# Performance work log

Measured on AMD Instinct MI355X. Metric: run time of the kernel, lower is better.

Reference implementation:

```python
import jax, jax.numpy as jnp
import numpy as np

BLOCK = 4096  # bitsandbytes blockwise-quantization block size


def setup_inputs() -> dict:
    key = jax.random.key(0)
    k_x, k_w, k_a, k_c, k_b = jax.random.split(key, 5)
    out_features, in_features = 16384, 4096
    numel = out_features * in_features
    x = jax.random.normal(k_x, (2, 2048, in_features), dtype=jnp.float32)
    # int8 codes stored as indices into the 256-entry dequant table
    qweight = jax.random.randint(k_w, (out_features, in_features), 0, 256, dtype=jnp.int32)
    absmax = jax.random.uniform(k_a, (numel // BLOCK,), dtype=jnp.float32)
    code = jax.random.normal(k_c, (256,), dtype=jnp.float32)
    bias = jax.random.normal(k_b, (out_features,), dtype=jnp.float32)
    return {"x": x, "qweight": qweight, "absmax": absmax, "code": code, "bias": bias}


def reference(x, qweight, absmax, code, bias):
    # dequantize_blockwise: w[i] = code[q[i]] * absmax[i // BLOCK]
    out_f, in_f = qweight.shape
    w = (code[qweight.reshape(-1)].reshape(-1, BLOCK) * absmax[:, None]).reshape(out_f, in_f)
    # F.linear(x, W, b) = x @ W^T + b
    return jnp.einsum("bsi,oi->bso", x, w) + bias
```

## Files before the change

kernel.cpp:

```cpp
#include <hip/hip_runtime.h>
#include <hip/hip_bf16.h>


typedef __bf16 bf16x8 __attribute__((ext_vector_type(8)));
typedef __bf16 bf16x4 __attribute__((ext_vector_type(4)));
typedef float  f32x4  __attribute__((ext_vector_type(4)));

#define GLD_LDS(gp, lp) \
    __builtin_amdgcn_global_load_lds((const __attribute__((address_space(1))) void*)(gp), \
                                     (__attribute__((address_space(3))) void*)(lp), 16, 0, 0)

static constexpr int M = 4096;
static constexpr int N = 16384;
static constexpr int K = 4096;
static constexpr int BM = 256;
static constexpr int BN = 256;
static constexpr int BK = 64;
static constexpr int NT = K / BK;
static constexpr int LDS_BYTES = 2 * 2 * 256 * BK * 2;

__global__ __launch_bounds__(256) void dequant_w(const int4* __restrict__ q4,
                                                 const float* __restrict__ code,
                                                 const float* __restrict__ absmax,
                                                 bf16x4* __restrict__ W)
{
    __shared__ float lc[256];
    lc[threadIdx.x] = code[threadIdx.x];
    __syncthreads();
    unsigned gid = blockIdx.x * 256u + threadIdx.x;
    int4 qv = q4[gid];
    float am = absmax[gid >> 10];
    bf16x4 w;
    w[0] = (__bf16)(lc[qv.x] * am);
    w[1] = (__bf16)(lc[qv.y] * am);
    w[2] = (__bf16)(lc[qv.z] * am);
    w[3] = (__bf16)(lc[qv.w] * am);
    W[gid] = w;
}

__global__ __launch_bounds__(256) void cvt_x(const float4* __restrict__ x,
                                             bf16x4* __restrict__ xb)
{
    unsigned gid = blockIdx.x * 256u + threadIdx.x;
    float4 v = x[gid];
    bf16x4 o;
    o[0] = (__bf16)v.x;
    o[1] = (__bf16)v.y;
    o[2] = (__bf16)v.z;
    o[3] = (__bf16)v.w;
    xb[gid] = o;
}


__device__ __forceinline__ void stage_half(const __bf16* gp, char* ldsbase, int h, int tid)
{
    GLD_LDS(gp + (size_t)(h * 128) * K,      ldsbase + h * 16384 +        tid * 16);
    GLD_LDS(gp + (size_t)(h * 128 + 64) * K, ldsbase + h * 16384 + 8192 + tid * 16);
}

__device__ __forceinline__ void tile_step(const __bf16*& agn, const __bf16*& bgn,
                                          const char* cA, const char* cB,
                                          char* nA, char* nB, bool pf, int tid,
                                          int baseA, int baseB, f32x4 (&acc)[8][4])
{
    if (pf) {
        stage_half(agn, nA, 0, tid);
        stage_half(agn, nA, 1, tid);
        stage_half(bgn, nB, 0, tid);
        asm volatile("s_waitcnt vmcnt(6)" ::: "memory");
    } else {
        asm volatile("s_waitcnt vmcnt(0)" ::: "memory");
    }
    __builtin_amdgcn_s_barrier();

    if (pf) {
        stage_half(bgn, nB, 1, tid);
        agn += BK;
        bgn += BK;
    }

    bf16x8 bfr[4][2], af[2][2];
#pragma unroll
    for (int ni = 0; ni < 4; ++ni) {
        bfr[ni][0] = *(const bf16x8*)(cB + (baseB + ni * 2048));
        bfr[ni][1] = *(const bf16x8*)(cB + ((baseB + ni * 2048) ^ 64));
    }
    af[0][0] = *(const bf16x8*)(cA + baseA);
    af[0][1] = *(const bf16x8*)(cA + (baseA ^ 64));
    af[1][0] = *(const bf16x8*)(cA + (baseA + 2048));
    af[1][1] = *(const bf16x8*)(cA + ((baseA + 2048) ^ 64));

    __builtin_amdgcn_s_barrier();
    __builtin_amdgcn_s_setprio(1);
#pragma unroll
    for (int kk = 0; kk < 2; ++kk)
#pragma unroll
        for (int i = 0; i < 2; ++i)
#pragma unroll
            for (int ni = 0; ni < 4; ++ni)
                acc[i][ni] = __builtin_amdgcn_mfma_f32_16x16x32_bf16(
                    af[i][kk], bfr[ni][kk], acc[i][ni], 0, 0, 0);
    __builtin_amdgcn_s_setprio(0);
    __builtin_amdgcn_s_barrier();

#pragma unroll
    for (int p = 1; p < 4; ++p) {
        af[0][0] = *(const bf16x8*)(cA + (baseA + (2 * p) * 2048));
        af[0][1] = *(const bf16x8*)(cA + ((baseA + (2 * p) * 2048) ^ 64));
        af[1][0] = *(const bf16x8*)(cA + (baseA + (2 * p + 1) * 2048));
        af[1][1] = *(const bf16x8*)(cA + ((baseA + (2 * p + 1) * 2048) ^ 64));
        __builtin_amdgcn_s_barrier();
        __builtin_amdgcn_s_setprio(1);
#pragma unroll
        for (int kk = 0; kk < 2; ++kk)
#pragma unroll
            for (int i = 0; i < 2; ++i)
#pragma unroll
                for (int ni = 0; ni < 4; ++ni)
                    acc[2 * p + i][ni] = __builtin_amdgcn_mfma_f32_16x16x32_bf16(
                        af[i][kk], bfr[ni][kk], acc[2 * p + i][ni], 0, 0, 0);
        __builtin_amdgcn_s_setprio(0);
        __builtin_amdgcn_s_barrier();
    }
}

__global__ __launch_bounds__(512, 2) void gemm_bt_bias(const __bf16* __restrict__ A,
                                                       const __bf16* __restrict__ B,
                                                       const float* __restrict__ bias,
                                                       float* __restrict__ C)
{
    extern __shared__ char lds[];
    const int tid  = threadIdx.x;
    const int lane = tid & 63;
    const int wave = tid >> 6;
    const int wm = wave >> 2;
    const int wn = wave & 3;

    const int cpx  = (int)gridDim.x >> 3;
    const int flat = ((int)blockIdx.x & 7) * cpx + ((int)blockIdx.x >> 3);
    const int bm = (flat & (M / BM - 1)) * BM;
    const int bn = (flat / (M / BM)) * BN;

    const int r0 = tid >> 3;
    const int cs = (tid & 7) ^ (r0 & 7);
    const __bf16* ag = A + (size_t)(bm + r0) * K + cs * 8;
    const __bf16* bg = B + (size_t)(bn + r0) * K + cs * 8;

    char* const ldsA0 = lds;
    char* const ldsB0 = lds + 32768;
    char* const ldsA1 = lds + 65536;
    char* const ldsB1 = lds + 98304;

    const int swz   = ((lane >> 4) ^ (lane & 7)) << 4;
    const int baseA = (wm * 128 + (lane & 15)) * 128 + swz;
    const int baseB = (wn * 64  + (lane & 15)) * 128 + swz;

    f32x4 acc[8][4] = {};

    stage_half(ag, ldsA0, 0, tid);
    stage_half(ag, ldsA0, 1, tid);
    stage_half(bg, ldsB0, 0, tid);
    stage_half(bg, ldsB0, 1, tid);

    const __bf16* agn = ag + BK;
    const __bf16* bgn = bg + BK;

    for (int t2 = 0; t2 < NT; t2 += 2) {
        tile_step(agn, bgn, ldsA0, ldsB0, ldsA1, ldsB1, true,         tid, baseA, baseB, acc);
        tile_step(agn, bgn, ldsA1, ldsB1, ldsA0, ldsB0, t2 + 2 < NT,  tid, baseA, baseB, acc);
    }

    const int cn = lane & 15;
    const int rq = (lane >> 4) * 4;
#pragma unroll
    for (int ni = 0; ni < 4; ++ni) {
        const int n = bn + wn * 64 + ni * 16 + cn;
        const float bv = bias[n];
#pragma unroll
        for (int mi = 0; mi < 8; ++mi) {
#pragma unroll
            for (int r = 0; r < 4; ++r) {
                const int m = bm + wm * 128 + mi * 16 + rq + r;
                C[(size_t)m * N + n] = acc[mi][ni][r] + bv;
            }
        }
    }
}

extern "C" void kernel_launch(void* const* d_in, const int* in_sizes, int n_in,
                              void* d_out, int out_size, void* d_ws, size_t ws_size,
                              hipStream_t stream)
{
    const float* x      = (const float*)d_in[0];
    const int*   qw     = (const int*)d_in[1];
    const float* absmax = (const float*)d_in[2];
    const float* code   = (const float*)d_in[3];
    const float* bias   = (const float*)d_in[4];
    float* out = (float*)d_out;

    __bf16* Wb = (__bf16*)d_ws;
    __bf16* Xb = (__bf16*)((char*)d_ws + (size_t)N * K * sizeof(__bf16));

    static bool attr_set = false;
    if (!attr_set) {
        (void)hipFuncSetAttribute((const void*)gemm_bt_bias,
                                  hipFuncAttributeMaxDynamicSharedMemorySize, LDS_BYTES);
        attr_set = true;
    }

    dequant_w<<<(N * (long long)K) / 4 / 256, 256, 0, stream>>>(
        (const int4*)qw, code, absmax, (bf16x4*)Wb);

    cvt_x<<<(M * (long long)K) / 4 / 256, 256, 0, stream>>>(
        (const float4*)x, (bf16x4*)Xb);

    gemm_bt_bias<<<dim3((M / BM) * (N / BN)), dim3(512), LDS_BYTES, stream>>>(
        Xb, Wb, bias, out);
}
```

Before: 1.006 ms.

## Split GEMM tile into quadrants with interleaved staging, and widen prep kernels

```diff
diff --git a/kernel.cpp b/kernel.cpp
--- a/kernel.cpp
+++ b/kernel.cpp
@@ -3,7 +3,6 @@
 
 
 typedef __bf16 bf16x8 __attribute__((ext_vector_type(8)));
-typedef __bf16 bf16x4 __attribute__((ext_vector_type(4)));
 typedef float  f32x4  __attribute__((ext_vector_type(4)));
 
 #define GLD_LDS(gp, lp) \
@@ -17,111 +16,66 @@
 static constexpr int BN = 256;
 static constexpr int BK = 64;
 static constexpr int NT = K / BK;
-static constexpr int LDS_BYTES = 2 * 2 * 256 * BK * 2;
+static constexpr int LDS_BYTES = 131072;
 
 __global__ __launch_bounds__(256) void dequant_w(const int4* __restrict__ q4,
                                                  const float* __restrict__ code,
                                                  const float* __restrict__ absmax,
-                                                 bf16x4* __restrict__ W)
+                                                 bf16x8* __restrict__ W)
 {
     __shared__ float lc[256];
     lc[threadIdx.x] = code[threadIdx.x];
     __syncthreads();
-    unsigned gid = blockIdx.x * 256u + threadIdx.x;
-    int4 qv = q4[gid];
-    float am = absmax[gid >> 10];
-    bf16x4 w;
-    w[0] = (__bf16)(lc[qv.x] * am);
-    w[1] = (__bf16)(lc[qv.y] * am);
-    w[2] = (__bf16)(lc[qv.z] * am);
-    w[3] = (__bf16)(lc[qv.w] * am);
-    W[gid] = w;
+    const unsigned total  = (unsigned)((unsigned long long)N * K / 8);
+    const unsigned stride = gridDim.x * 256u;
+    for (unsigned gid = blockIdx.x * 256u + threadIdx.x; gid < total; gid += stride) {
+        int4 q0 = q4[2u * gid];
+        int4 q1 = q4[2u * gid + 1u];
+        float am = absmax[gid >> 9];
+        bf16x8 w;
+        w[0] = (__bf16)(lc[q0.x] * am);
+        w[1] = (__bf16)(lc[q0.y] * am);
+        w[2] = (__bf16)(lc[q0.z] * am);
+        w[3] = (__bf16)(lc[q0.w] * am);
+        w[4] = (__bf16)(lc[q1.x] * am);
+        w[5] = (__bf16)(lc[q1.y] * am);
+        w[6] = (__bf16)(lc[q1.z] * am);
+        w[7] = (__bf16)(lc[q1.w] * am);
+        W[gid] = w;
+    }
 }
 
 __global__ __launch_bounds__(256) void cvt_x(const float4* __restrict__ x,
-                                             bf16x4* __restrict__ xb)
-{
-    unsigned gid = blockIdx.x * 256u + threadIdx.x;
-    float4 v = x[gid];
-    bf16x4 o;
-    o[0] = (__bf16)v.x;
-    o[1] = (__bf16)v.y;
-    o[2] = (__bf16)v.z;
-    o[3] = (__bf16)v.w;
-    xb[gid] = o;
-}
-
-
-__device__ __forceinline__ void stage_half(const __bf16* gp, char* ldsbase, int h, int tid)
-{
-    GLD_LDS(gp + (size_t)(h * 128) * K,      ldsbase + h * 16384 +        tid * 16);
-    GLD_LDS(gp + (size_t)(h * 128 + 64) * K, ldsbase + h * 16384 + 8192 + tid * 16);
-}
-
-__device__ __forceinline__ void tile_step(const __bf16*& agn, const __bf16*& bgn,
-                                          const char* cA, const char* cB,
-                                          char* nA, char* nB, bool pf, int tid,
-                                          int baseA, int baseB, f32x4 (&acc)[8][4])
-{
-    if (pf) {
-        stage_half(agn, nA, 0, tid);
-        stage_half(agn, nA, 1, tid);
-        stage_half(bgn, nB, 0, tid);
-        asm volatile("s_waitcnt vmcnt(6)" ::: "memory");
-    } else {
-        asm volatile("s_waitcnt vmcnt(0)" ::: "memory");
-    }
-    __builtin_amdgcn_s_barrier();
-
-    if (pf) {
-        stage_half(bgn, nB, 1, tid);
-        agn += BK;
-        bgn += BK;
-    }
-
-    bf16x8 bfr[4][2], af[2][2];
-#pragma unroll
-    for (int ni = 0; ni < 4; ++ni) {
-        bfr[ni][0] = *(const bf16x8*)(cB + (baseB + ni * 2048));
-        bfr[ni][1] = *(const bf16x8*)(cB + ((baseB + ni * 2048) ^ 64));
-    }
-    af[0][0] = *(const bf16x8*)(cA + baseA);
-    af[0][1] = *(const bf16x8*)(cA + (baseA ^ 64));
-    af[1][0] = *(const bf16x8*)(cA + (baseA + 2048));
-    af[1][1] = *(const bf16x8*)(cA + ((baseA + 2048) ^ 64));
-
-    __builtin_amdgcn_s_barrier();
+                                             bf16x8* __restrict__ xb)
+{
+    const unsigned total  = (unsigned)((unsigned long long)M * K / 8);
+    const unsigned stride = gridDim.x * 256u;
+    for (unsigned gid = blockIdx.x * 256u + threadIdx.x; gid < total; gid += stride) {
+        float4 a = x[2u * gid];
+        float4 b = x[2u * gid + 1u];
+        bf16x8 o;
+        o[0] = (__bf16)a.x; o[1] = (__bf16)a.y; o[2] = (__bf16)a.z; o[3] = (__bf16)a.w;
+        o[4] = (__bf16)b.x; o[5] = (__bf16)b.y; o[6] = (__bf16)b.z; o[7] = (__bf16)b.w;
+        xb[gid] = o;
+    }
+}
+
+
+template<int MH, int NH>
+__device__ __forceinline__ void mfma_quad(f32x4 (&acc)[8][4],
+                                          const bf16x8 (&af)[4][2],
+                                          const bf16x8 (&bf)[2][2])
+{
     __builtin_amdgcn_s_setprio(1);
 #pragma unroll
     for (int kk = 0; kk < 2; ++kk)
 #pragma unroll
-        for (int i = 0; i < 2; ++i)
-#pragma unroll
-            for (int ni = 0; ni < 4; ++ni)
-                acc[i][ni] = __builtin_amdgcn_mfma_f32_16x16x32_bf16(
-                    af[i][kk], bfr[ni][kk], acc[i][ni], 0, 0, 0);
+        for (int mi = 0; mi < 4; ++mi)
+#pragma unroll
+            for (int ni = 0; ni < 2; ++ni)
+                acc[MH * 4 + mi][NH * 2 + ni] = __builtin_amdgcn_mfma_f32_16x16x32_bf16(
+                    af[mi][kk], bf[ni][kk], acc[MH * 4 + mi][NH * 2 + ni], 0, 0, 0);
     __builtin_amdgcn_s_setprio(0);
-    __builtin_amdgcn_s_barrier();
-
-#pragma unroll
-    for (int p = 1; p < 4; ++p) {
-        af[0][0] = *(const bf16x8*)(cA + (baseA + (2 * p) * 2048));
-        af[0][1] = *(const bf16x8*)(cA + ((baseA + (2 * p) * 2048) ^ 64));
-        af[1][0] = *(const bf16x8*)(cA + (baseA + (2 * p + 1) * 2048));
-        af[1][1] = *(const bf16x8*)(cA + ((baseA + (2 * p + 1) * 2048) ^ 64));
-        __builtin_amdgcn_s_barrier();
-        __builtin_amdgcn_s_setprio(1);
-#pragma unroll
-        for (int kk = 0; kk < 2; ++kk)
-#pragma unroll
-            for (int i = 0; i < 2; ++i)
-#pragma unroll
-                for (int ni = 0; ni < 4; ++ni)
-                    acc[2 * p + i][ni] = __builtin_amdgcn_mfma_f32_16x16x32_bf16(
-                        af[i][kk], bfr[ni][kk], acc[2 * p + i][ni], 0, 0, 0);
-        __builtin_amdgcn_s_setprio(0);
-        __builtin_amdgcn_s_barrier();
-    }
 }
 
 __global__ __launch_bounds__(512, 2) void gemm_bt_bias(const __bf16* __restrict__ A,
@@ -143,31 +97,94 @@
 
     const int r0 = tid >> 3;
     const int cs = (tid & 7) ^ (r0 & 7);
+    const int b_r0 = (r0 & 31) + (r0 >> 5) * 64;
+
     const __bf16* ag = A + (size_t)(bm + r0) * K + cs * 8;
-    const __bf16* bg = B + (size_t)(bn + r0) * K + cs * 8;
+    const __bf16* bg = B + (size_t)(bn + b_r0) * K + cs * 8;
 
     char* const ldsA0 = lds;
     char* const ldsB0 = lds + 32768;
     char* const ldsA1 = lds + 65536;
     char* const ldsB1 = lds + 98304;
-
-    const int swz   = ((lane >> 4) ^ (lane & 7)) << 4;
-    const int baseA = (wm * 128 + (lane & 15)) * 128 + swz;
-    const int baseB = (wn * 64  + (lane & 15)) * 128 + swz;
+    const int ldst = tid * 16;
+
+    auto stageA = [&](char* dst, int h, size_t kn) {
+        GLD_LDS(ag + kn + (size_t)(h * 64) * K,       dst + h * 16384 + ldst);
+        GLD_LDS(ag + kn + (size_t)(h * 64 + 128) * K, dst + h * 16384 + 8192 + ldst);
+    };
+    auto stageB = [&](char* dst, int h, size_t kn) {
+        GLD_LDS(bg + kn + (size_t)(h * 32) * K,       dst + h * 16384 + ldst);
+        GLD_LDS(bg + kn + (size_t)(h * 32 + 128) * K, dst + h * 16384 + 8192 + ldst);
+    };
+
+    const int fr  = lane & 15;
+    const int swz = ((lane >> 4) ^ (lane & 7)) << 4;
+    const int aoff = (wm * 64 + fr) * 128 + swz;
+    const int boff = (wn * 32 + fr) * 128 + swz;
+
+    auto loadA = [&](const char* cA, int mh, bf16x8 (&af)[4][2]) {
+        const int base = mh * 16384 + aoff;
+#pragma unroll
+        for (int mi = 0; mi < 4; ++mi) {
+            af[mi][0] = *(const bf16x8*)(cA + (base + mi * 2048));
+            af[mi][1] = *(const bf16x8*)(cA + ((base + mi * 2048) ^ 64));
+        }
+    };
+    auto loadB = [&](const char* cB, int nh, bf16x8 (&bf)[2][2]) {
+        const int base = nh * 16384 + boff;
+#pragma unroll
+        for (int ni = 0; ni < 2; ++ni) {
+            bf[ni][0] = *(const bf16x8*)(cB + (base + ni * 2048));
+            bf[ni][1] = *(const bf16x8*)(cB + ((base + ni * 2048) ^ 64));
+        }
+    };
 
     f32x4 acc[8][4] = {};
 
-    stage_half(ag, ldsA0, 0, tid);
-    stage_half(ag, ldsA0, 1, tid);
-    stage_half(bg, ldsB0, 0, tid);
-    stage_half(bg, ldsB0, 1, tid);
-
-    const __bf16* agn = ag + BK;
-    const __bf16* bgn = bg + BK;
-
-    for (int t2 = 0; t2 < NT; t2 += 2) {
-        tile_step(agn, bgn, ldsA0, ldsB0, ldsA1, ldsB1, true,         tid, baseA, baseB, acc);
-        tile_step(agn, bgn, ldsA1, ldsB1, ldsA0, ldsB0, t2 + 2 < NT,  tid, baseA, baseB, acc);
+    stageA(ldsA0, 0, 0);
+    stageB(ldsB0, 0, 0);
+    stageB(ldsB0, 1, 0);
+    stageA(ldsA0, 1, 0);
+    asm volatile("s_waitcnt vmcnt(4)" ::: "memory");
+    __builtin_amdgcn_s_barrier();
+
+    auto tile_body = [&](const char* cA, const char* cB, char* nA, char* nB,
+                         bool pf, size_t kn) {
+        bf16x8 af[4][2], bf[2][2];
+        if (pf) stageA(nA, 0, kn);
+        loadA(cA, 0, af);
+        loadB(cB, 0, bf);
+        if (pf) asm volatile("s_waitcnt vmcnt(4)" ::: "memory");
+        else    asm volatile("s_waitcnt vmcnt(0)" ::: "memory");
+        __builtin_amdgcn_s_barrier();
+        mfma_quad<0, 0>(acc, af, bf);
+        if (pf) stageB(nB, 0, kn);
+        loadB(cB, 1, bf);
+        if (pf) {
+            asm volatile("s_waitcnt vmcnt(4)" ::: "memory");
+            __builtin_amdgcn_s_barrier();
+        }
+        mfma_quad<0, 1>(acc, af, bf);
+        if (pf) stageB(nB, 1, kn);
+        loadA(cA, 1, af);
+        loadB(cB, 0, bf);
+        if (pf) {
+            asm volatile("s_waitcnt vmcnt(4)" ::: "memory");
+            __builtin_amdgcn_s_barrier();
+        }
+        mfma_quad<1, 0>(acc, af, bf);
+        if (pf) stageA(nA, 1, kn);
+        loadB(cB, 1, bf);
+        if (pf) {
+            asm volatile("s_waitcnt vmcnt(4)" ::: "memory");
+            __builtin_amdgcn_s_barrier();
+        }
+        mfma_quad<1, 1>(acc, af, bf);
+    };
+
+    for (int t = 0; t < NT; t += 2) {
+        tile_body(ldsA0, ldsB0, ldsA1, ldsB1, true,        (size_t)(t + 1) * BK);
+        tile_body(ldsA1, ldsB1, ldsA0, ldsB0, t + 2 < NT,  (size_t)(t + 2) * BK);
     }
 
     const int cn = lane & 15;
@@ -208,11 +225,8 @@
         attr_set = true;
     }
 
-    dequant_w<<<(N * (long long)K) / 4 / 256, 256, 0, stream>>>(
-        (const int4*)qw, code, absmax, (bf16x4*)Wb);
-
-    cvt_x<<<(M * (long long)K) / 4 / 256, 256, 0, stream>>>(
-        (const float4*)x, (bf16x4*)Xb);
+    dequant_w<<<2048, 256, 0, stream>>>((const int4*)qw, code, absmax, (bf16x8*)Wb);
+    cvt_x<<<2048, 256, 0, stream>>>((const float4*)x, (bf16x8*)Xb);
 
     gemm_bt_bias<<<dim3((M / BM) * (N / BN)), dim3(512), LDS_BYTES, stream>>>(
         Xb, Wb, bias, out);
```

Result: no change. 994.1 us (-1.1%).
